# Kernel tuning notes

Measured on AMD Instinct MI355X. Metric: run time of the kernel, lower is better.

The kernel has to match this reference:

```python
import jax, jax.numpy as jnp
import numpy as np

B, T, D, L, H = 4096, 200, 128, 64, 128  # n_traj, time steps, input_dim, latent_dim, n_units


def _lin(key, fan_in, fan_out):
    s = 1.0 / np.sqrt(fan_in)
    kw, kb = jax.random.split(key)
    w = jax.random.uniform(kw, (fan_in, fan_out), jnp.float32, -s, s)
    b = jax.random.uniform(kb, (fan_out,), jnp.float32, -s, s)
    return w, b


def setup_inputs() -> dict:
    key = jax.random.key(0)
    ks = jax.random.split(key, 8)
    data = jax.random.normal(ks[0], (B, T, D), jnp.float32)
    time_steps = jax.random.uniform(ks[1], (T,), jnp.float32)
    cin = 2 * L + D
    ug_w1, ug_b1 = _lin(ks[2], cin, H)
    ug_w2, ug_b2 = _lin(ks[3], H, L)
    rg_w1, rg_b1 = _lin(ks[4], cin, H)
    rg_w2, rg_b2 = _lin(ks[5], H, L)
    ns_w1, ns_b1 = _lin(ks[6], cin, H)
    ns_w2, ns_b2 = _lin(ks[7], H, 2 * L)
    return dict(data=data, time_steps=time_steps,
                ug_w1=ug_w1, ug_b1=ug_b1, ug_w2=ug_w2, ug_b2=ug_b2,
                rg_w1=rg_w1, rg_b1=rg_b1, rg_w2=rg_w2, rg_b2=rg_b2,
                ns_w1=ns_w1, ns_b1=ns_b1, ns_w2=ns_w2, ns_b2=ns_b2)


def reference(data, time_steps,
              ug_w1, ug_b1, ug_w2, ug_b2,
              rg_w1, rg_b1, rg_w2, rg_b2,
              ns_w1, ns_b1, ns_w2, ns_b2):
    # GRUUnit (latent-ODE style): gates are 2-layer MLPs (Tanh hidden) over
    # concat([y_mean, y_logvar, x]); update/reset end in Sigmoid, new_state
    # net emits 2L (mean, |std|).
    def step(carry, x):  # x: [B, D]
        y, s = carry  # each [B, L]
        h = jnp.concatenate([y, s, x], axis=-1)  # [B, 2L+D]
        u = jax.nn.sigmoid(jnp.tanh(h @ ug_w1 + ug_b1) @ ug_w2 + ug_b2)
        r = jax.nn.sigmoid(jnp.tanh(h @ rg_w1 + rg_b1) @ rg_w2 + rg_b2)
        hc = jnp.concatenate([y * r, s * r, x], axis=-1)
        ns = jnp.tanh(hc @ ns_w1 + ns_b1) @ ns_w2 + ns_b2  # [B, 2L]
        new_mean = ns[:, :L]
        new_std = jnp.abs(ns[:, L:])
        y2 = (1.0 - u) * new_mean + u * y
        s2 = (1.0 - u) * new_std + u * s
        return (y2, s2), None

    y0 = jnp.zeros((data.shape[0], L), data.dtype)
    s0 = jnp.zeros((data.shape[0], L), data.dtype)
    xs = jnp.transpose(data, (1, 0, 2))  # [T, B, D]; scan over time
    (yT, sT), _ = jax.lax.scan(step, (y0, s0), xs)
    return yT, sT
```

## Files before the change

### kernel.cpp

```cpp
#include <hip/hip_runtime.h>
#include <hip/hip_bf16.h>


#define NB 4096
#define NT 200
#define ND 128
#define NL 64
#define NH 128

typedef __bf16 bf16;
typedef __attribute__((ext_vector_type(8))) __bf16 bf16x8;
typedef __attribute__((ext_vector_type(4))) __bf16 bf16x4;
typedef __attribute__((ext_vector_type(4))) float f32x4;

#define BAR() asm volatile("s_waitcnt lgkmcnt(0)\n\ts_barrier" ::: "memory")

__device__ __forceinline__ f32x4 mfma16(bf16x8 a, bf16x8 b, f32x4 c){
    return __builtin_amdgcn_mfma_f32_16x16x32_bf16(a, b, c, 0, 0, 0);
}

__device__ __forceinline__ float fast_tanh(float x){
    float e = __expf(2.f * x);
    return 1.f - 2.f * __builtin_amdgcn_rcpf(e + 1.f);
}
__device__ __forceinline__ float fast_sigmoid(float x){
    float e = __expf(-x);
    return __builtin_amdgcn_rcpf(1.f + e);
}

__device__ __forceinline__ bf16x4 tanh4_bf16(f32x4 a, float4 b){
    bf16x4 o;
    o[0] = (bf16)fast_tanh(a[0] + b.x);
    o[1] = (bf16)fast_tanh(a[1] + b.y);
    o[2] = (bf16)fast_tanh(a[2] + b.z);
    o[3] = (bf16)fast_tanh(a[3] + b.w);
    return o;
}

__global__ __launch_bounds__(512, 2)
void vae_rnn(const float* __restrict__ data,
             const float* __restrict__ ug_w1, const float* __restrict__ ug_b1,
             const float* __restrict__ ug_w2, const float* __restrict__ ug_b2,
             const float* __restrict__ rg_w1, const float* __restrict__ rg_b1,
             const float* __restrict__ rg_w2, const float* __restrict__ rg_b2,
             const float* __restrict__ ns_w1, const float* __restrict__ ns_b1,
             const float* __restrict__ ns_w2, const float* __restrict__ ns_b2,
             float* __restrict__ out)
{
    __shared__ __align__(16) char h_lds [16 * 512];
    __shared__ __align__(16) char t_lds [16 * 512];
    __shared__ __align__(16) char tn_lds[16 * 256];
    __shared__ float u_lds [16][68];
    __shared__ float ys_lds[16][132];

    const int tid  = threadIdx.x;
    const int wave = tid >> 6;
    const int lane = tid & 63;
    const int lq   = lane >> 4;
    const int lc   = lane & 15;
    const int sw   = (lc & 7) << 4;
    const int row0 = blockIdx.x * 16;

    bf16x8 wA[16]; float4 bA[2];
    #pragma unroll
    for (int j = 0; j < 2; ++j){
        int c = wave*32 + j*16 + lc;
        const float* W  = (c < 128) ? ug_w1 : rg_w1;
        int n = c & 127;
        int fb = (wave*32 + j*16 + lq*4) & 127;
        const float* bb = ((wave*32 + j*16) < 128) ? ug_b1 : rg_b1;
        bA[j] = make_float4(bb[fb], bb[fb+1], bb[fb+2], bb[fb+3]);
        #pragma unroll
        for (int kt = 0; kt < 8; ++kt){
            int k0 = kt*32 + lq*8;
            bf16x8 f;
            #pragma unroll
            for (int e = 0; e < 8; ++e) f[e] = (bf16)W[(k0 + e)*NH + n];
            wA[kt*2 + j] = f;
        }
    }
    bf16x8 wB[4]; float4 bB;
    {
        const float* W  = (wave < 4) ? ug_w2 : rg_w2;
        const float* bb = (wave < 4) ? ug_b2 : rg_b2;
        int n  = (wave & 3)*16 + lc;
        int fb = (wave & 3)*16 + lq*4;
        bB = make_float4(bb[fb], bb[fb+1], bb[fb+2], bb[fb+3]);
        #pragma unroll
        for (int kt = 0; kt < 4; ++kt){
            int k0 = kt*32 + lq*8;
            bf16x8 f;
            #pragma unroll
            for (int e = 0; e < 8; ++e) f[e] = (bf16)W[(k0 + e)*NL + n];
            wB[kt] = f;
        }
    }
    bf16x8 wC[8]; float4 bC;
    {
        int n  = wave*16 + lc;
        int fb = wave*16 + lq*4;
        bC = make_float4(ns_b1[fb], ns_b1[fb+1], ns_b1[fb+2], ns_b1[fb+3]);
        #pragma unroll
        for (int kt = 0; kt < 8; ++kt){
            int k0 = kt*32 + lq*8;
            bf16x8 f;
            #pragma unroll
            for (int e = 0; e < 8; ++e) f[e] = (bf16)ns_w1[(k0 + e)*NH + n];
            wC[kt] = f;
        }
    }
    bf16x8 wD[4]; float4 bD;
    {
        int n  = wave*16 + lc;
        int fb = wave*16 + lq*4;
        bD = make_float4(ns_b2[fb], ns_b2[fb+1], ns_b2[fb+2], ns_b2[fb+3]);
        #pragma unroll
        for (int kt = 0; kt < 4; ++kt){
            int k0 = kt*32 + lq*8;
            bf16x8 f;
            #pragma unroll
            for (int e = 0; e < 8; ++e) f[e] = (bf16)ns_w2[(k0 + e)*NH + n];
            wD[kt] = f;
        }
    }

    for (int i = tid; i < 16*132; i += 512) (&ys_lds[0][0])[i] = 0.f;
    const int xr = tid >> 5;
    const int xc = (tid & 31) << 2;
    const int swx = (xr & 7) << 4;
    const float* xbase = data + (size_t)(row0 + xr) * (NT * ND) + xc;
    {
        float4 x0 = *(const float4*)xbase;
        bf16x4 z = { (bf16)0.f, (bf16)0.f, (bf16)0.f, (bf16)0.f };
        bf16x4 xb = { (bf16)x0.x, (bf16)x0.y, (bf16)x0.z, (bf16)x0.w };
        *(bf16x4*)(h_lds + xr*512 + ((xc*2)       ^ swx)) = z;
        *(bf16x4*)(h_lds + xr*512 + (((128+xc)*2) ^ swx)) = xb;
    }
    BAR();

    #pragma unroll 1
    for (int t = 0; t < NT; ++t){
        int tn1 = (t + 1 < NT) ? (t + 1) : (NT - 1);
        float4 xnext = *(const float4*)(xbase + tn1*ND);

        bf16x8 xf[4];

        {
            f32x4 acc[2][2] = {};
            #pragma unroll
            for (int kt = 0; kt < 8; ++kt){
                bf16x8 av = *(const bf16x8*)(h_lds + lc*512 + ((kt*64 + lq*16) ^ sw));
                if (kt >= 4) xf[kt-4] = av;
                acc[0][kt&1] = mfma16(wA[kt*2+0], av, acc[0][kt&1]);
                acc[1][kt&1] = mfma16(wA[kt*2+1], av, acc[1][kt&1]);
            }
            #pragma unroll
            for (int j = 0; j < 2; ++j){
                f32x4 a = acc[j][0] + acc[j][1];
                int f0 = wave*32 + j*16 + lq*4;
                *(bf16x4*)(t_lds + lc*512 + ((f0*2) ^ sw)) = tanh4_bf16(a, bA[j]);
            }
        }
        BAR();

        {
            float4 y4 = {}, s4 = {};
            int f0 = (wave & 3)*16 + lq*4;
            if (wave >= 4){
                y4 = *(const float4*)&ys_lds[lc][f0];
                s4 = *(const float4*)&ys_lds[lc][64 + f0];
            }
            f32x4 acc0 = {}, acc1 = {};
            const int off = (wave < 4) ? 0 : 256;
            #pragma unroll
            for (int kt = 0; kt < 4; ++kt){
                bf16x8 av = *(const bf16x8*)(t_lds + lc*512 + ((off + kt*64 + lq*16) ^ sw));
                if (kt & 1) acc1 = mfma16(wB[kt], av, acc1);
                else        acc0 = mfma16(wB[kt], av, acc0);
            }
            f32x4 acc = acc0 + acc1;
            float g0 = fast_sigmoid(acc[0] + bB.x);
            float g1 = fast_sigmoid(acc[1] + bB.y);
            float g2 = fast_sigmoid(acc[2] + bB.z);
            float g3 = fast_sigmoid(acc[3] + bB.w);
            if (wave < 4){
                *(float4*)&u_lds[lc][f0] = make_float4(g0, g1, g2, g3);
            } else {
                bf16x4 hy = { (bf16)(y4.x*g0), (bf16)(y4.y*g1), (bf16)(y4.z*g2), (bf16)(y4.w*g3) };
                bf16x4 hs = { (bf16)(s4.x*g0), (bf16)(s4.y*g1), (bf16)(s4.z*g2), (bf16)(s4.w*g3) };
                *(bf16x4*)(h_lds + lc*512 + ((f0*2)      ^ sw)) = hy;
                *(bf16x4*)(h_lds + lc*512 + (((64+f0)*2) ^ sw)) = hs;
            }
        }
        BAR();

        float4 u4, o4;
        {
            int fd = (wave & 3)*16 + lq*4;
            int sc = (wave >= 4) ? 64 : 0;
            u4 = *(const float4*)&u_lds[lc][fd];
            o4 = *(const float4*)&ys_lds[lc][sc + fd];

            f32x4 acc[2] = {};
            #pragma unroll
            for (int kt = 0; kt < 4; ++kt){
                bf16x8 av = *(const bf16x8*)(h_lds + lc*512 + ((kt*64 + lq*16) ^ sw));
                acc[kt&1] = mfma16(wC[kt], av, acc[kt&1]);
            }
            #pragma unroll
            for (int kt = 4; kt < 8; ++kt)
                acc[kt&1] = mfma16(wC[kt], xf[kt-4], acc[kt&1]);
            f32x4 a = acc[0] + acc[1];
            int f0 = wave*16 + lq*4;
            *(bf16x4*)(tn_lds + lc*256 + ((f0*2) ^ sw)) = tanh4_bf16(a, bC);
        }
        BAR();

        {
            f32x4 acc0 = {}, acc1 = {};
            #pragma unroll
            for (int kt = 0; kt < 4; ++kt){
                bf16x8 av = *(const bf16x8*)(tn_lds + lc*256 + ((kt*64 + lq*16) ^ sw));
                if (kt & 1) acc1 = mfma16(wD[kt], av, acc1);
                else        acc0 = mfma16(wD[kt], av, acc0);
            }
            f32x4 acc = acc0 + acc1;
            int f0 = (wave & 3)*16 + lq*4;
            int sc = (wave >= 4) ? 64 : 0;
            float v0 = acc[0] + bD.x, v1 = acc[1] + bD.y;
            float v2 = acc[2] + bD.z, v3 = acc[3] + bD.w;
            if (wave >= 4){ v0 = fabsf(v0); v1 = fabsf(v1); v2 = fabsf(v2); v3 = fabsf(v3); }
            float n0 = fmaf(u4.x, o4.x - v0, v0);
            float n1 = fmaf(u4.y, o4.y - v1, v1);
            float n2 = fmaf(u4.z, o4.z - v2, v2);
            float n3 = fmaf(u4.w, o4.w - v3, v3);
            *(float4*)&ys_lds[lc][sc + f0] = make_float4(n0, n1, n2, n3);
            bf16x4 hn = { (bf16)n0, (bf16)n1, (bf16)n2, (bf16)n3 };
            *(bf16x4*)(h_lds + lc*512 + (((sc + f0)*2) ^ sw)) = hn;
            bf16x4 xb = { (bf16)xnext.x, (bf16)xnext.y, (bf16)xnext.z, (bf16)xnext.w };
            *(bf16x4*)(h_lds + xr*512 + (((128+xc)*2) ^ swx)) = xb;
        }
        BAR();
    }

    {
        float4 v = *(const float4*)&ys_lds[xr][xc];
        size_t gr = (size_t)(row0 + xr);
        if (xc < 64) *(float4*)&out[gr*64 + xc] = v;
        else         *(float4*)&out[(size_t)NB*64 + gr*64 + (xc - 64)] = v;
    }
}

extern "C" void kernel_launch(void* const* d_in, const int* in_sizes, int n_in,
                              void* d_out, int out_size, void* d_ws, size_t ws_size,
                              hipStream_t stream) {
    const float* data  = (const float*)d_in[0];
    const float* ug_w1 = (const float*)d_in[2];
    const float* ug_b1 = (const float*)d_in[3];
    const float* ug_w2 = (const float*)d_in[4];
    const float* ug_b2 = (const float*)d_in[5];
    const float* rg_w1 = (const float*)d_in[6];
    const float* rg_b1 = (const float*)d_in[7];
    const float* rg_w2 = (const float*)d_in[8];
    const float* rg_b2 = (const float*)d_in[9];
    const float* ns_w1 = (const float*)d_in[10];
    const float* ns_b1 = (const float*)d_in[11];
    const float* ns_w2 = (const float*)d_in[12];
    const float* ns_b2 = (const float*)d_in[13];

    hipLaunchKernelGGL(vae_rnn, dim3(NB/16), dim3(512), 0, stream,
                       data, ug_w1, ug_b1, ug_w2, ug_b2,
                       rg_w1, rg_b1, rg_w2, rg_b2,
                       ns_w1, ns_b1, ns_w2, ns_b2,
                       (float*)d_out);
}
```

Measured before the change: 401.0 us.

## Halve waves per block, fold biases into accumulators, overlap x-part of new-state GEMM

Each 16-row block now runs 4 waves instead of 8, so every wave owns twice as many output tiles, with twice the weight fragments held in registers. Biases are preloaded into the MFMA accumulators instead of being added afterwards. The x-input part of the new-state first layer is issued during the gate stage, so the phase after the barrier only handles the reset-scaled state. LDS rows are padded to 528/272 bytes instead of XOR swizzling. The intent is fewer waves contending at each barrier and more per-wave MFMA work to hide latency, at the cost of higher register pressure and lower occupancy (launch bounds 256,1).

Result: slower. 616.4 us (+53.7%).

```diff
diff --git a/kernel.cpp b/kernel.cpp
--- a/kernel.cpp
+++ b/kernel.cpp
@@ -5,8 +5,6 @@
 #define NB 4096
 #define NT 200
 #define ND 128
-#define NL 64
-#define NH 128
 
 typedef __bf16 bf16;
 typedef __attribute__((ext_vector_type(8))) __bf16 bf16x8;
@@ -18,26 +16,26 @@
 __device__ __forceinline__ f32x4 mfma16(bf16x8 a, bf16x8 b, f32x4 c){
     return __builtin_amdgcn_mfma_f32_16x16x32_bf16(a, b, c, 0, 0, 0);
 }
-
 __device__ __forceinline__ float fast_tanh(float x){
     float e = __expf(2.f * x);
     return 1.f - 2.f * __builtin_amdgcn_rcpf(e + 1.f);
 }
 __device__ __forceinline__ float fast_sigmoid(float x){
-    float e = __expf(-x);
-    return __builtin_amdgcn_rcpf(1.f + e);
-}
-
-__device__ __forceinline__ bf16x4 tanh4_bf16(f32x4 a, float4 b){
+    return __builtin_amdgcn_rcpf(1.f + __expf(-x));
+}
+__device__ __forceinline__ bf16x4 tanh4(f32x4 a){
     bf16x4 o;
-    o[0] = (bf16)fast_tanh(a[0] + b.x);
-    o[1] = (bf16)fast_tanh(a[1] + b.y);
-    o[2] = (bf16)fast_tanh(a[2] + b.z);
-    o[3] = (bf16)fast_tanh(a[3] + b.w);
+    o[0] = (bf16)fast_tanh(a[0]);
+    o[1] = (bf16)fast_tanh(a[1]);
+    o[2] = (bf16)fast_tanh(a[2]);
+    o[3] = (bf16)fast_tanh(a[3]);
     return o;
 }
-
-__global__ __launch_bounds__(512, 2)
+__device__ __forceinline__ f32x4 finit(float4 b){
+    f32x4 r; r[0]=b.x; r[1]=b.y; r[2]=b.z; r[3]=b.w; return r;
+}
+
+__global__ __launch_bounds__(256, 1)
 void vae_rnn(const float* __restrict__ data,
              const float* __restrict__ ug_w1, const float* __restrict__ ug_b1,
              const float* __restrict__ ug_w2, const float* __restrict__ ug_b2,
@@ -47,207 +45,245 @@
              const float* __restrict__ ns_w2, const float* __restrict__ ns_b2,
              float* __restrict__ out)
 {
-    __shared__ __align__(16) char h_lds [16 * 512];
-    __shared__ __align__(16) char t_lds [16 * 512];
-    __shared__ __align__(16) char tn_lds[16 * 256];
+    __shared__ __align__(16) char h_lds [16 * 528];
+    __shared__ __align__(16) char t_lds [16 * 528];
+    __shared__ __align__(16) char tn_lds[16 * 272];
     __shared__ float u_lds [16][68];
     __shared__ float ys_lds[16][132];
 
     const int tid  = threadIdx.x;
-    const int wave = tid >> 6;
+    const int w    = tid >> 6;
     const int lane = tid & 63;
     const int lq   = lane >> 4;
     const int lc   = lane & 15;
-    const int sw   = (lc & 7) << 4;
     const int row0 = blockIdx.x * 16;
-
-    bf16x8 wA[16]; float4 bA[2];
-    #pragma unroll
-    for (int j = 0; j < 2; ++j){
-        int c = wave*32 + j*16 + lc;
-        const float* W  = (c < 128) ? ug_w1 : rg_w1;
-        int n = c & 127;
-        int fb = (wave*32 + j*16 + lq*4) & 127;
-        const float* bb = ((wave*32 + j*16) < 128) ? ug_b1 : rg_b1;
-        bA[j] = make_float4(bb[fb], bb[fb+1], bb[fb+2], bb[fb+3]);
-        #pragma unroll
-        for (int kt = 0; kt < 8; ++kt){
-            int k0 = kt*32 + lq*8;
-            bf16x8 f;
-            #pragma unroll
-            for (int e = 0; e < 8; ++e) f[e] = (bf16)W[(k0 + e)*NH + n];
-            wA[kt*2 + j] = f;
-        }
-    }
-    bf16x8 wB[4]; float4 bB;
-    {
-        const float* W  = (wave < 4) ? ug_w2 : rg_w2;
-        const float* bb = (wave < 4) ? ug_b2 : rg_b2;
-        int n  = (wave & 3)*16 + lc;
-        int fb = (wave & 3)*16 + lq*4;
-        bB = make_float4(bb[fb], bb[fb+1], bb[fb+2], bb[fb+3]);
-        #pragma unroll
-        for (int kt = 0; kt < 4; ++kt){
-            int k0 = kt*32 + lq*8;
-            bf16x8 f;
-            #pragma unroll
-            for (int e = 0; e < 8; ++e) f[e] = (bf16)W[(k0 + e)*NL + n];
-            wB[kt] = f;
-        }
-    }
-    bf16x8 wC[8]; float4 bC;
-    {
-        int n  = wave*16 + lc;
-        int fb = wave*16 + lq*4;
-        bC = make_float4(ns_b1[fb], ns_b1[fb+1], ns_b1[fb+2], ns_b1[fb+3]);
-        #pragma unroll
-        for (int kt = 0; kt < 8; ++kt){
-            int k0 = kt*32 + lq*8;
-            bf16x8 f;
-            #pragma unroll
-            for (int e = 0; e < 8; ++e) f[e] = (bf16)ns_w1[(k0 + e)*NH + n];
-            wC[kt] = f;
-        }
-    }
-    bf16x8 wD[4]; float4 bD;
-    {
-        int n  = wave*16 + lc;
-        int fb = wave*16 + lq*4;
-        bD = make_float4(ns_b2[fb], ns_b2[fb+1], ns_b2[fb+2], ns_b2[fb+3]);
-        #pragma unroll
-        for (int kt = 0; kt < 4; ++kt){
-            int k0 = kt*32 + lq*8;
-            bf16x8 f;
-            #pragma unroll
-            for (int e = 0; e < 8; ++e) f[e] = (bf16)ns_w2[(k0 + e)*NH + n];
-            wD[kt] = f;
-        }
-    }
-
-    for (int i = tid; i < 16*132; i += 512) (&ys_lds[0][0])[i] = 0.f;
-    const int xr = tid >> 5;
-    const int xc = (tid & 31) << 2;
-    const int swx = (xr & 7) << 4;
-    const float* xbase = data + (size_t)(row0 + xr) * (NT * ND) + xc;
-    {
-        float4 x0 = *(const float4*)xbase;
-        bf16x4 z = { (bf16)0.f, (bf16)0.f, (bf16)0.f, (bf16)0.f };
-        bf16x4 xb = { (bf16)x0.x, (bf16)x0.y, (bf16)x0.z, (bf16)x0.w };
-        *(bf16x4*)(h_lds + xr*512 + ((xc*2)       ^ swx)) = z;
-        *(bf16x4*)(h_lds + xr*512 + (((128+xc)*2) ^ swx)) = xb;
+    const bool RU  = (w < 2);
+    const int  w2  = RU ? w : (w - 2);
+
+    bf16x8 wA[32]; float4 bA[4];
+    {
+        const float* W  = RU ? ug_w1 : rg_w1;
+        const float* bb = RU ? ug_b1 : rg_b1;
+        #pragma unroll
+        for (int j = 0; j < 4; ++j){
+            int n  = (w*64 + j*16 + lc) & 127;
+            int fb = (w*64 + j*16 + lq*4) & 127;
+            bA[j] = make_float4(bb[fb], bb[fb+1], bb[fb+2], bb[fb+3]);
+            #pragma unroll
+            for (int kt = 0; kt < 8; ++kt){
+                bf16x8 f;
+                #pragma unroll
+                for (int e = 0; e < 8; ++e) f[e] = (bf16)W[(kt*32 + lq*8 + e)*128 + n];
+                wA[kt*4 + j] = f;
+            }
+        }
+    }
+    bf16x8 wB[8]; float4 bB[2];
+    {
+        const float* W  = RU ? ug_w2 : rg_w2;
+        const float* bb = RU ? ug_b2 : rg_b2;
+        #pragma unroll
+        for (int j = 0; j < 2; ++j){
+            int n  = w2*32 + j*16 + lc;
+            int fb = w2*32 + j*16 + lq*4;
+            bB[j] = make_float4(bb[fb], bb[fb+1], bb[fb+2], bb[fb+3]);
+            #pragma unroll
+            for (int kt = 0; kt < 4; ++kt){
+                bf16x8 f;
+                #pragma unroll
+                for (int e = 0; e < 8; ++e) f[e] = (bf16)W[(kt*32 + lq*8 + e)*64 + n];
+                wB[kt*2 + j] = f;
+            }
+        }
+    }
+    bf16x8 wC[16]; float4 bC[2];
+    {
+        #pragma unroll
+        for (int j = 0; j < 2; ++j){
+            int n  = w*32 + j*16 + lc;
+            int fb = w*32 + j*16 + lq*4;
+            bC[j] = make_float4(ns_b1[fb], ns_b1[fb+1], ns_b1[fb+2], ns_b1[fb+3]);
+            #pragma unroll
+            for (int kt = 0; kt < 8; ++kt){
+                bf16x8 f;
+                #pragma unroll
+                for (int e = 0; e < 8; ++e) f[e] = (bf16)ns_w1[(kt*32 + lq*8 + e)*128 + n];
+                wC[kt*2 + j] = f;
+            }
+        }
+    }
+    const int nb0 = RU ? (w*32) : (64 + w2*32);
+    bf16x8 wD[8]; float4 bD[2];
+    {
+        #pragma unroll
+        for (int j = 0; j < 2; ++j){
+            int n  = nb0 + j*16 + lc;
+            int fb = nb0 + j*16 + lq*4;
+            bD[j] = make_float4(ns_b2[fb], ns_b2[fb+1], ns_b2[fb+2], ns_b2[fb+3]);
+            #pragma unroll
+            for (int kt = 0; kt < 4; ++kt){
+                bf16x8 f;
+                #pragma unroll
+                for (int e = 0; e < 8; ++e) f[e] = (bf16)ns_w2[(kt*32 + lq*8 + e)*128 + n];
+                wD[kt*2 + j] = f;
+            }
+        }
+    }
+
+    const char* h_rd  = h_lds  + lc*528 + lq*16;
+    char*       t_wr  = t_lds  + lc*528 + w*128 + lq*8;
+    const char* t_rd  = t_lds  + lc*528 + lq*16 + (RU ? 0 : 256);
+    char*       tn_wr = tn_lds + lc*272 + w*64 + lq*8;
+    const char* tn_rd = tn_lds + lc*272 + lq*16;
+
+    for (int i = tid; i < 16*132; i += 256) (&ys_lds[0][0])[i] = 0.f;
+    const int xr  = tid >> 4;
+    const int xci = tid & 15;
+    const float* xbase = data + (size_t)(row0 + xr) * (NT * ND) + xci*8;
+    {
+        bf16x8 z = {};
+        *(bf16x8*)(h_lds + xr*528 + xci*16) = z;
+        float4 a0 = *(const float4*)(xbase);
+        float4 a1 = *(const float4*)(xbase + 4);
+        bf16x8 xb = { (bf16)a0.x,(bf16)a0.y,(bf16)a0.z,(bf16)a0.w,
+                      (bf16)a1.x,(bf16)a1.y,(bf16)a1.z,(bf16)a1.w };
+        *(bf16x8*)(h_lds + xr*528 + 256 + xci*16) = xb;
     }
     BAR();
+
+    const int cB = w2*32 + lq*4;
+    const int cD = nb0 + lq*4;
+    const int uD = (nb0 & 63) + lq*4;
 
     #pragma unroll 1
     for (int t = 0; t < NT; ++t){
         int tn1 = (t + 1 < NT) ? (t + 1) : (NT - 1);
-        float4 xnext = *(const float4*)(xbase + tn1*ND);
-
-        bf16x8 xf[4];
-
+        float4 xn0 = *(const float4*)(xbase + tn1*ND);
+        float4 xn1 = *(const float4*)(xbase + tn1*ND + 4);
+
+        bf16x8 xf0, xf1, xf2, xf3;
+        f32x4 a0 = finit(bA[0]), a1 = finit(bA[1]), a2 = finit(bA[2]), a3 = finit(bA[3]);
+        #pragma unroll
+        for (int kt = 0; kt < 8; ++kt){
+            bf16x8 av = *(const bf16x8*)(h_rd + kt*64);
+            if (kt == 4) xf0 = av;
+            if (kt == 5) xf1 = av;
+            if (kt == 6) xf2 = av;
+            if (kt == 7) xf3 = av;
+            a0 = mfma16(wA[kt*4+0], av, a0);
+            a1 = mfma16(wA[kt*4+1], av, a1);
+            a2 = mfma16(wA[kt*4+2], av, a2);
+            a3 = mfma16(wA[kt*4+3], av, a3);
+        }
+        *(bf16x4*)(t_wr +  0) = tanh4(a0);
+        *(bf16x4*)(t_wr + 32) = tanh4(a1);
+        *(bf16x4*)(t_wr + 64) = tanh4(a2);
+        *(bf16x4*)(t_wr + 96) = tanh4(a3);
+        BAR();
+
+        float4 y4a, s4a, y4b, s4b;
+        if (!RU){
+            y4a = *(const float4*)&ys_lds[lc][cB];
+            s4a = *(const float4*)&ys_lds[lc][64 + cB];
+            y4b = *(const float4*)&ys_lds[lc][cB + 16];
+            s4b = *(const float4*)&ys_lds[lc][80 + cB];
+        }
+        f32x4 b0 = finit(bB[0]), b1 = finit(bB[1]);
+        f32x4 cx0 = finit(bC[0]), cx1 = finit(bC[1]);
+        #pragma unroll
+        for (int kt = 0; kt < 4; ++kt){
+            bf16x8 tv = *(const bf16x8*)(t_rd + kt*64);
+            b0 = mfma16(wB[kt*2+0], tv, b0);
+            b1 = mfma16(wB[kt*2+1], tv, b1);
+        }
+        cx0 = mfma16(wC[ 8], xf0, cx0);  cx1 = mfma16(wC[ 9], xf0, cx1);
+        cx0 = mfma16(wC[10], xf1, cx0);  cx1 = mfma16(wC[11], xf1, cx1);
+        cx0 = mfma16(wC[12], xf2, cx0);  cx1 = mfma16(wC[13], xf2, cx1);
+        cx0 = mfma16(wC[14], xf3, cx0);  cx1 = mfma16(wC[15], xf3, cx1);
         {
-            f32x4 acc[2][2] = {};
-            #pragma unroll
-            for (int kt = 0; kt < 8; ++kt){
-                bf16x8 av = *(const bf16x8*)(h_lds + lc*512 + ((kt*64 + lq*16) ^ sw));
-                if (kt >= 4) xf[kt-4] = av;
-                acc[0][kt&1] = mfma16(wA[kt*2+0], av, acc[0][kt&1]);
-                acc[1][kt&1] = mfma16(wA[kt*2+1], av, acc[1][kt&1]);
-            }
-            #pragma unroll
-            for (int j = 0; j < 2; ++j){
-                f32x4 a = acc[j][0] + acc[j][1];
-                int f0 = wave*32 + j*16 + lq*4;
-                *(bf16x4*)(t_lds + lc*512 + ((f0*2) ^ sw)) = tanh4_bf16(a, bA[j]);
+            float g00 = fast_sigmoid(b0[0]), g01 = fast_sigmoid(b0[1]);
+            float g02 = fast_sigmoid(b0[2]), g03 = fast_sigmoid(b0[3]);
+            float g10 = fast_sigmoid(b1[0]), g11 = fast_sigmoid(b1[1]);
+            float g12 = fast_sigmoid(b1[2]), g13 = fast_sigmoid(b1[3]);
+            if (RU){
+                *(float4*)&u_lds[lc][cB]      = make_float4(g00, g01, g02, g03);
+                *(float4*)&u_lds[lc][cB + 16] = make_float4(g10, g11, g12, g13);
+            } else {
+                bf16x4 hy0 = { (bf16)(y4a.x*g00), (bf16)(y4a.y*g01), (bf16)(y4a.z*g02), (bf16)(y4a.w*g03) };
+                bf16x4 hs0 = { (bf16)(s4a.x*g00), (bf16)(s4a.y*g01), (bf16)(s4a.z*g02), (bf16)(s4a.w*g03) };
+                bf16x4 hy1 = { (bf16)(y4b.x*g10), (bf16)(y4b.y*g11), (bf16)(y4b.z*g12), (bf16)(y4b.w*g13) };
+                bf16x4 hs1 = { (bf16)(s4b.x*g10), (bf16)(s4b.y*g11), (bf16)(s4b.z*g12), (bf16)(s4b.w*g13) };
+                char* hw = h_lds + lc*528 + 2*cB;
+                *(bf16x4*)(hw +   0) = hy0;
+                *(bf16x4*)(hw +  32) = hy1;
+                *(bf16x4*)(hw + 128) = hs0;
+                *(bf16x4*)(hw + 160) = hs1;
             }
         }
         BAR();
 
+        #pragma unroll
+        for (int kt = 0; kt < 4; ++kt){
+            bf16x8 hv = *(const bf16x8*)(h_rd + kt*64);
+            cx0 = mfma16(wC[kt*2+0], hv, cx0);
+            cx1 = mfma16(wC[kt*2+1], hv, cx1);
+        }
+        *(bf16x4*)(tn_wr +  0) = tanh4(cx0);
+        *(bf16x4*)(tn_wr + 32) = tanh4(cx1);
+        BAR();
+
         {
-            float4 y4 = {}, s4 = {};
-            int f0 = (wave & 3)*16 + lq*4;
-            if (wave >= 4){
-                y4 = *(const float4*)&ys_lds[lc][f0];
-                s4 = *(const float4*)&ys_lds[lc][64 + f0];
-            }
-            f32x4 acc0 = {}, acc1 = {};
-            const int off = (wave < 4) ? 0 : 256;
+            float4 u4a = *(const float4*)&u_lds[lc][uD];
+            float4 u4b = *(const float4*)&u_lds[lc][uD + 16];
+            float4 o4a = *(const float4*)&ys_lds[lc][cD];
+            float4 o4b = *(const float4*)&ys_lds[lc][cD + 16];
+            f32x4 d0 = finit(bD[0]), d1 = finit(bD[1]);
             #pragma unroll
             for (int kt = 0; kt < 4; ++kt){
-                bf16x8 av = *(const bf16x8*)(t_lds + lc*512 + ((off + kt*64 + lq*16) ^ sw));
-                if (kt & 1) acc1 = mfma16(wB[kt], av, acc1);
-                else        acc0 = mfma16(wB[kt], av, acc0);
-            }
-            f32x4 acc = acc0 + acc1;
-            float g0 = fast_sigmoid(acc[0] + bB.x);
-            float g1 = fast_sigmoid(acc[1] + bB.y);
-            float g2 = fast_sigmoid(acc[2] + bB.z);
-            float g3 = fast_sigmoid(acc[3] + bB.w);
-            if (wave < 4){
-                *(float4*)&u_lds[lc][f0] = make_float4(g0, g1, g2, g3);
-            } else {
-                bf16x4 hy = { (bf16)(y4.x*g0), (bf16)(y4.y*g1), (bf16)(y4.z*g2), (bf16)(y4.w*g3) };
-                bf16x4 hs = { (bf16)(s4.x*g0), (bf16)(s4.y*g1), (bf16)(s4.z*g2), (bf16)(s4.w*g3) };
-                *(bf16x4*)(h_lds + lc*512 + ((f0*2)      ^ sw)) = hy;
-                *(bf16x4*)(h_lds + lc*512 + (((64+f0)*2) ^ sw)) = hs;
-            }
+                bf16x8 tv = *(const bf16x8*)(tn_rd + kt*64);
+                d0 = mfma16(wD[kt*2+0], tv, d0);
+                d1 = mfma16(wD[kt*2+1], tv, d1);
+            }
+            float v00 = d0[0], v01 = d0[1], v02 = d0[2], v03 = d0[3];
+            float v10 = d1[0], v11 = d1[1], v12 = d1[2], v13 = d1[3];
+            if (!RU){
+                v00 = fabsf(v00); v01 = fabsf(v01); v02 = fabsf(v02); v03 = fabsf(v03);
+                v10 = fabsf(v10); v11 = fabsf(v11); v12 = fabsf(v12); v13 = fabsf(v13);
+            }
+            float n00 = fmaf(u4a.x, o4a.x - v00, v00);
+            float n01 = fmaf(u4a.y, o4a.y - v01, v01);
+            float n02 = fmaf(u4a.z, o4a.z - v02, v02);
+            float n03 = fmaf(u4a.w, o4a.w - v03, v03);
+            float n10 = fmaf(u4b.x, o4b.x - v10, v10);
+            float n11 = fmaf(u4b.y, o4b.y - v11, v11);
+            float n12 = fmaf(u4b.z, o4b.z - v12, v12);
+            float n13 = fmaf(u4b.w, o4b.w - v13, v13);
+            *(float4*)&ys_lds[lc][cD]      = make_float4(n00, n01, n02, n03);
+            *(float4*)&ys_lds[lc][cD + 16] = make_float4(n10, n11, n12, n13);
+            bf16x4 h0 = { (bf16)n00, (bf16)n01, (bf16)n02, (bf16)n03 };
+            bf16x4 h1 = { (bf16)n10, (bf16)n11, (bf16)n12, (bf16)n13 };
+            char* hw = h_lds + lc*528 + 2*cD;
+            *(bf16x4*)(hw +  0) = h0;
+            *(bf16x4*)(hw + 32) = h1;
+            bf16x8 xb = { (bf16)xn0.x,(bf16)xn0.y,(bf16)xn0.z,(bf16)xn0.w,
+                          (bf16)xn1.x,(bf16)xn1.y,(bf16)xn1.z,(bf16)xn1.w };
+            *(bf16x8*)(h_lds + xr*528 + 256 + xci*16) = xb;
         }
         BAR();
-
-        float4 u4, o4;
-        {
-            int fd = (wave & 3)*16 + lq*4;
-            int sc = (wave >= 4) ? 64 : 0;
-            u4 = *(const float4*)&u_lds[lc][fd];
-            o4 = *(const float4*)&ys_lds[lc][sc + fd];
-
-            f32x4 acc[2] = {};
-            #pragma unroll
-            for (int kt = 0; kt < 4; ++kt){
-                bf16x8 av = *(const bf16x8*)(h_lds + lc*512 + ((kt*64 + lq*16) ^ sw));
-                acc[kt&1] = mfma16(wC[kt], av, acc[kt&1]);
-            }
-            #pragma unroll
-            for (int kt = 4; kt < 8; ++kt)
-                acc[kt&1] = mfma16(wC[kt], xf[kt-4], acc[kt&1]);
-            f32x4 a = acc[0] + acc[1];
-            int f0 = wave*16 + lq*4;
-            *(bf16x4*)(tn_lds + lc*256 + ((f0*2) ^ sw)) = tanh4_bf16(a, bC);
-        }
-        BAR();
-
-        {
-            f32x4 acc0 = {}, acc1 = {};
-            #pragma unroll
-            for (int kt = 0; kt < 4; ++kt){
-                bf16x8 av = *(const bf16x8*)(tn_lds + lc*256 + ((kt*64 + lq*16) ^ sw));
-                if (kt & 1) acc1 = mfma16(wD[kt], av, acc1);
-                else        acc0 = mfma16(wD[kt], av, acc0);
-            }
-            f32x4 acc = acc0 + acc1;
-            int f0 = (wave & 3)*16 + lq*4;
-            int sc = (wave >= 4) ? 64 : 0;
-            float v0 = acc[0] + bD.x, v1 = acc[1] + bD.y;
-            float v2 = acc[2] + bD.z, v3 = acc[3] + bD.w;
-            if (wave >= 4){ v0 = fabsf(v0); v1 = fabsf(v1); v2 = fabsf(v2); v3 = fabsf(v3); }
-            float n0 = fmaf(u4.x, o4.x - v0, v0);
-            float n1 = fmaf(u4.y, o4.y - v1, v1);
-            float n2 = fmaf(u4.z, o4.z - v2, v2);
-            float n3 = fmaf(u4.w, o4.w - v3, v3);
-            *(float4*)&ys_lds[lc][sc + f0] = make_float4(n0, n1, n2, n3);
-            bf16x4 hn = { (bf16)n0, (bf16)n1, (bf16)n2, (bf16)n3 };
-            *(bf16x4*)(h_lds + lc*512 + (((sc + f0)*2) ^ sw)) = hn;
-            bf16x4 xb = { (bf16)xnext.x, (bf16)xnext.y, (bf16)xnext.z, (bf16)xnext.w };
-            *(bf16x4*)(h_lds + xr*512 + (((128+xc)*2) ^ swx)) = xb;
-        }
-        BAR();
-    }
-
-    {
-        float4 v = *(const float4*)&ys_lds[xr][xc];
+    }
+
+    {
+        int xc8 = xci * 8;
+        float4 v0 = *(const float4*)&ys_lds[xr][xc8];
+        float4 v1 = *(const float4*)&ys_lds[xr][xc8 + 4];
         size_t gr = (size_t)(row0 + xr);
-        if (xc < 64) *(float4*)&out[gr*64 + xc] = v;
-        else         *(float4*)&out[(size_t)NB*64 + gr*64 + (xc - 64)] = v;
+        if (xc8 < 64){
+            *(float4*)&out[gr*64 + xc8]     = v0;
+            *(float4*)&out[gr*64 + xc8 + 4] = v1;
+        } else {
+            *(float4*)&out[(size_t)NB*64 + gr*64 + (xc8 - 64)]     = v0;
+            *(float4*)&out[(size_t)NB*64 + gr*64 + (xc8 - 64) + 4] = v1;
+        }
     }
 }
 
@@ -268,7 +304,7 @@
     const float* ns_w2 = (const float*)d_in[12];
     const float* ns_b2 = (const float*)d_in[13];
 
-    hipLaunchKernelGGL(vae_rnn, dim3(NB/16), dim3(512), 0, stream,
+    hipLaunchKernelGGL(vae_rnn, dim3(NB/16), dim3(256), 0, stream,
                        data, ug_w1, ug_b1, ug_w2, ug_b2,
                        rg_w1, rg_b1, rg_w2, rg_b2,
                        ns_w1, ns_b1, ns_w2, ns_b2,
```
